# Performance work log

Hardware: AMD Instinct MI355X
Metric: run time of the kernel (lower is better)

The kernel has to match this reference:

```python
import jax, jax.numpy as jnp
import numpy as np

S, B, E, H, V, L = 128, 64, 512, 1024, 10000, 2


def setup_inputs() -> dict:
    key = jax.random.key(0)
    ks = jax.random.split(key, 10)
    s = 0.02  # weight scale ~ uniform(-k,k) magnitude
    return {
        "inputs": jax.random.randint(ks[0], (S, B), 0, V),
        "hidden": jnp.zeros((L, B, H), jnp.float32),
        "emb": jax.random.normal(ks[1], (V, E), jnp.float32) * 0.1,
        "Wx0": jax.random.normal(ks[2], (3, H, E), jnp.float32) * s,
        "Uh0": jax.random.normal(ks[3], (3, H, H), jnp.float32) * s,
        "b0": jax.random.normal(ks[4], (3, H), jnp.float32) * s,
        "Wx1": jax.random.normal(ks[5], (3, H, H), jnp.float32) * s,
        "Uh1": jax.random.normal(ks[6], (3, H, H), jnp.float32) * s,
        "b1": jax.random.normal(ks[7], (3, H), jnp.float32) * s,
        "Wd": jax.random.normal(ks[8], (V, H), jnp.float32) * 0.1,
        "bd": jnp.zeros((V,), jnp.float32),
    }


def _gru_cell(xp, h, U, b):
    # xp: (3,B,H) precomputed input projections in [r,z,h] order
    r = jax.nn.sigmoid(xp[0] + h @ U[0].T + b[0])
    z = jax.nn.sigmoid(xp[1] + h @ U[1].T + b[1])
    h_tilde = jnp.tanh(xp[2] + (r * h) @ U[2].T + b[2])
    return (1.0 - z) * h + z * h_tilde


def reference(inputs, hidden, emb, Wx0, Uh0, b0, Wx1, Uh1, b1, Wd, bd):
    x_embs = emb[inputs]                                   # [S,B,E]
    # precompute layer-0 input projections across all timesteps
    xa0 = jnp.einsum("sbe,goe->sgbo", x_embs, Wx0)        # [S,3,B,H]

    def step(carry, xa0_t):
        h0, h1 = carry
        h0n = _gru_cell(xa0_t, h0, Uh0, b0)
        xp1 = jnp.einsum("bk,gok->gbo", h0n, Wx1)          # [3,B,H]
        h1n = _gru_cell(xp1, h1, Uh1, b1)
        return (h0n, h1n), h1n

    (h0f, h1f), hs1 = jax.lax.scan(step, (hidden[0], hidden[1]), xa0)
    logits = jnp.einsum("sbh,vh->sbv", hs1, Wd) + bd       # [S,B,V]
    return logits, jnp.stack([h0f, h1f])
```

## Files before the change

kernel.cpp:

```cpp
#include <hip/hip_runtime.h>
#include <hip/hip_bf16.h>

#define SLEN 128
#define BAT 64
#define EDIM 512
#define HDIM 1024
#define VOC 10000
#define VPAD 10112
#define NWG_REC 256
#define TPB_REC 512

typedef short v8s __attribute__((ext_vector_type(8)));
typedef float v4f __attribute__((ext_vector_type(4)));
typedef unsigned short u16;

__device__ __forceinline__ u16 f2bf(float f) {
  unsigned u = __float_as_uint(f);
  u += 0x7fffu + ((u >> 16) & 1u);
  return (u16)(u >> 16);
}
__device__ __forceinline__ float bf2f(u16 b) {
  return __uint_as_float(((unsigned)b) << 16);
}
__device__ __forceinline__ float sigm(float x) { return 1.f / (1.f + __expf(-x)); }
__device__ __forceinline__ float tanh_f(float x) { return 1.f - 2.f / (1.f + __expf(2.f * x)); }

__device__ __forceinline__ void st_f32(float* p, float v) {
  __hip_atomic_store(p, v, __ATOMIC_RELAXED, __HIP_MEMORY_SCOPE_AGENT);
}
__device__ __forceinline__ float ld_f32(const float* p) {
  return __hip_atomic_load(p, __ATOMIC_RELAXED, __HIP_MEMORY_SCOPE_AGENT);
}
__device__ __forceinline__ float ld_bf16(const unsigned* base, int elem) {
  unsigned pr = __hip_atomic_load(base + (elem >> 1), __ATOMIC_RELAXED, __HIP_MEMORY_SCOPE_AGENT);
  return bf2f((u16)((elem & 1) ? (pr >> 16) : (pr & 0xffffu)));
}
__device__ __forceinline__ void st_bf16_pair(unsigned* base, int elem, u16 val, int l) {
  unsigned p = (unsigned)__shfl_xor((int)val, 1);
  if ((l & 1) == 0)
    __hip_atomic_store(base + (elem >> 1), (unsigned)val | (p << 16),
                       __ATOMIC_RELAXED, __HIP_MEMORY_SCOPE_AGENT);
}

__device__ __forceinline__ v4f gemm_staged(const char* Asrc, char* stage,
                                           const char* bb, int swz,
                                           int t, int rg, int lr, int lk2) {
  const char* gp = Asrc + (t >> 3) * 2048 + (t & 7) * 16;
  char* wp = stage + (t >> 3) * 128 + (((t & 7) * 16) ^ (((t >> 3) & 7) << 4));
  const char* rp = stage + (rg * 16 + lr) * 128;
  v4f acc{0.f, 0.f, 0.f, 0.f};
  v8s sreg[3];
  asm volatile("global_load_dwordx4 %0, %1, off sc0 sc1" : "=v"(sreg[0]) : "v"(gp));
  asm volatile("global_load_dwordx4 %0, %1, off offset:128 sc0 sc1" : "=v"(sreg[1]) : "v"(gp));
  asm volatile("global_load_dwordx4 %0, %1, off offset:256 sc0 sc1" : "=v"(sreg[2]) : "v"(gp));
  asm volatile("s_waitcnt vmcnt(2)" ::: "memory");
  __builtin_amdgcn_sched_barrier(0);
  *(v8s*)wp = sreg[0];
  __syncthreads();
#pragma unroll
  for (int c = 0; c < 16; ++c) {
    if (c < 13)
      asm volatile("global_load_dwordx4 %0, %1, off offset:%2 sc0 sc1"
                   : "=v"(sreg[c % 3]) : "v"(gp), "i"((c + 3) * 128));
    if (c < 15) {
      if (c < 13)       asm volatile("s_waitcnt vmcnt(2)" ::: "memory");
      else if (c == 13) asm volatile("s_waitcnt vmcnt(1)" ::: "memory");
      else              asm volatile("s_waitcnt vmcnt(0)" ::: "memory");
      __builtin_amdgcn_sched_barrier(0);
      *(v8s*)(wp + ((c + 1) & 1) * 8192) = sreg[(c + 1) % 3];
    }
    const char* buf = rp + (c & 1) * 8192;
#pragma unroll
    for (int ls = 0; ls < 2; ++ls) {
      v8s a = *(const v8s*)(buf + ((ls * 64 + lk2) ^ swz));
      v8s b = *(const v8s*)(bb + (((c * 2 + ls) * 64 + lk2) ^ swz));
      acc = __builtin_amdgcn_mfma_f32_16x16x32_bf16(a, b, acc, 0, 0, 0);
    }
    __syncthreads();
  }
  return acc;
}

#define POLL(COND)                                   \
  do {                                               \
    if (t < 64) {                                    \
      for (;;) {                                     \
        bool ok_ = (COND);                           \
        if (__all(ok_)) break;                       \
        __builtin_amdgcn_s_sleep(1);                 \
      }                                              \
    }                                                \
    __syncthreads();                                 \
  } while (0)

#define FENCE_FLAG(FIDX)                                                        \
  do {                                                                          \
    asm volatile("s_waitcnt vmcnt(0) lgkmcnt(0)" ::: "memory");                 \
    __syncthreads();                                                            \
    if (t == 0)                                                                 \
      __hip_atomic_store(&bar[FIDX], T + 1, __ATOMIC_RELAXED,                   \
                         __HIP_MEMORY_SCOPE_AGENT);                             \
  } while (0)

__global__ void __launch_bounds__(TPB_REC, 2) k_recur(
    const u16* __restrict__ Uh0b, const u16* __restrict__ Wx1b, const u16* __restrict__ Uh1b,
    const float* __restrict__ b0, const float* __restrict__ b1,
    const u16* __restrict__ xa0,
    float* __restrict__ h0f, u16* __restrict__ h0b,
    float* __restrict__ h1f, u16* __restrict__ h1b,
    u16* __restrict__ a2, float* __restrict__ z0,
    u16* __restrict__ a5, float* __restrict__ z1,
    u16* __restrict__ xp1,
    u16* __restrict__ hs1,
    float* __restrict__ outh,
    int* __restrict__ bar) {
  extern __shared__ char smem[];
  const int wg = blockIdx.x;
  const int t = threadIdx.x;
  const int w = t >> 6;
  const int l = t & 63;
  const int lr = l & 15;
  const int lk2 = (l >> 4) * 16;
  const int rg = w >> 1, cg = w & 1;
  const int rbase = rg * 16 + ((l >> 4) << 2);
  const int swz = (lr & 7) << 4;
  char* stage = smem + 131072;

  unsigned* a2u  = (unsigned*)a2;
  unsigned* a5u  = (unsigned*)a5;
  unsigned* h0bu = (unsigned*)h0b;
  unsigned* h1bu = (unsigned*)h1b;
  unsigned* xpu  = (unsigned*)xp1;

  auto lf = [&](int i) {
    return __hip_atomic_load(&bar[i], __ATOMIC_RELAXED, __HIP_MEMORY_SCOPE_AGENT);
  };

  {
    const u16* w1src; int w1row0;
    if (wg < 64)       { w1src = Uh0b; w1row0 = wg * 32; }
    else if (wg < 96)  { w1src = Uh0b; w1row0 = 2048 + (wg - 64) * 32; }
    else if (wg < 192) { w1src = Wx1b; w1row0 = (wg - 96) * 32; }
    else               { w1src = Uh1b; w1row0 = (wg - 192) * 32; }
    for (int i = t; i < 4096; i += TPB_REC) {
      int c = i >> 7, j = i & 127;
      v8s v = *(const v8s*)(w1src + (size_t)(w1row0 + c) * HDIM + j * 8);
      *(v8s*)(smem + c * 2048 + ((j * 16) ^ ((c & 7) << 4))) = v;
    }
    if (wg >= 64 && wg < 96) {
      int w2row0 = 2048 + (wg - 64) * 32;
      for (int i = t; i < 4096; i += TPB_REC) {
        int c = i >> 7, j = i & 127;
        v8s v = *(const v8s*)(Uh1b + (size_t)(w2row0 + c) * HDIM + j * 8);
        *(v8s*)(smem + 65536 + c * 2048 + ((j * 16) ^ ((c & 7) << 4))) = v;
      }
    }
    __syncthreads();
  }

  const char* bb1 = smem + (cg * 16 + lr) * 2048;
  const char* bb2 = smem + 65536 + (cg * 16 + lr) * 2048;

  if (wg < 64) {
    const int g = wg >> 5;
    const int o = (wg * 32 + cg * 16 + lr) & 1023;
    const float bias = b0[g * HDIM + o];
    for (int T = 0; T <= SLEN + 1; ++T) {
      if (T < SLEN) {
        if (T >= 1) POLL(lf(64 + (t & 31)) >= T);
        const int pr = (T - 1) & 1, pw = T & 1;
        float xv[4], hv[4];
#pragma unroll
        for (int r = 0; r < 4; ++r) {
          int b = rbase + r;
          xv[r] = bf2f(xa0[((T * 3 + g) * BAT + b) * HDIM + o]);
          if (g == 0) hv[r] = ld_f32(h0f + pr * 65536 + b * HDIM + o);
        }
        v4f acc = gemm_staged((const char*)(h0b + pr * 65536), stage, bb1, swz, t, rg, lr, lk2);
#pragma unroll
        for (int r = 0; r < 4; ++r) {
          int b = rbase + r;
          float s = sigm(acc[r] + xv[r] + bias);
          if (g == 0) st_bf16_pair(a2u + pw * 32768, b * HDIM + o, f2bf(s * hv[r]), l);
          else        st_f32(z0 + pw * 65536 + b * HDIM + o, s);
        }
      }
      FENCE_FLAG(wg);
    }
  } else if (wg < 96) {
    const int j = wg - 64;
    const int o = j * 32 + cg * 16 + lr;
    const float bias0 = b0[2 * HDIM + o];
    const float bias1 = b1[2 * HDIM + o];
    for (int T = 0; T <= SLEN + 1; ++T) {
      if (T < SLEN) {
        POLL(lf(t & 31) >= T + 1);
        const int pr = (T - 1) & 1, pw = T & 1;
        float xv[4], hv[4];
#pragma unroll
        for (int r = 0; r < 4; ++r) {
          int b = rbase + r;
          xv[r] = bf2f(xa0[((T * 3 + 2) * BAT + b) * HDIM + o]);
          hv[r] = ld_f32(h0f + pr * 65536 + b * HDIM + o);
        }
        v4f acc = gemm_staged((const char*)(a2 + pw * 65536), stage, bb1, swz, t, rg, lr, lk2);
        POLL(lf(32 + (t & 31)) >= T + 1 && lf(128 + t) >= T && lf(192 + (t & 31)) >= T);
        float zv[4];
#pragma unroll
        for (int r = 0; r < 4; ++r) zv[r] = ld_f32(z0 + pw * 65536 + (rbase + r) * HDIM + o);
#pragma unroll
        for (int r = 0; r < 4; ++r) {
          int b = rbase + r;
          float ht = tanh_f(xv[r] + acc[r] + bias0);
          float hn = (1.f - zv[r]) * hv[r] + zv[r] * ht;
          st_f32(h0f + pw * 65536 + b * HDIM + o, hn);
          st_bf16_pair(h0bu + pw * 32768, b * HDIM + o, f2bf(hn), l);
          if (T == SLEN - 1) outh[b * HDIM + o] = hn;
        }
      }
      FENCE_FLAG(64 + j);
      if (T >= 2) {
        const int t5 = T - 2, p5 = t5 & 1, pm = (T - 3) & 1;
        POLL(lf(224 + t) >= T + 1);
        v4f acc = gemm_staged((const char*)(a5 + p5 * 65536), stage, bb2, swz, t, rg, lr, lk2);
        float pv[4], zv[4], hv[4];
#pragma unroll
        for (int r = 0; r < 4; ++r) {
          int b = rbase + r;
          pv[r] = ld_bf16(xpu + p5 * 98304, b * 3072 + 2048 + o);
          zv[r] = ld_f32(z1 + p5 * 65536 + b * HDIM + o);
          hv[r] = ld_f32(h1f + pm * 65536 + b * HDIM + o);
        }
#pragma unroll
        for (int r = 0; r < 4; ++r) {
          int b = rbase + r;
          float ht = tanh_f(pv[r] + acc[r] + bias1);
          float hn = (1.f - zv[r]) * hv[r] + zv[r] * ht;
          u16 hb = f2bf(hn);
          st_f32(h1f + p5 * 65536 + b * HDIM + o, hn);
          st_bf16_pair(h1bu + p5 * 32768, b * HDIM + o, hb, l);
          hs1[((size_t)t5 * BAT + b) * HDIM + o] = hb;
          if (t5 == SLEN - 1) outh[(size_t)BAT * HDIM + b * HDIM + o] = hn;
        }
      }
      FENCE_FLAG(96 + j);
    }
  } else if (wg < 192) {
    const int j = wg - 96;
    const int n = j * 32 + cg * 16 + lr;
    for (int T = 0; T <= SLEN + 1; ++T) {
      if (T >= 1 && T <= SLEN) {
        POLL(lf(64 + (t & 31)) >= T && lf(96 + (t & 31)) >= T);
        const int ts = T - 1, ps = ts & 1;
        v4f acc = gemm_staged((const char*)(h0b + ps * 65536), stage, bb1, swz, t, rg, lr, lk2);
        unsigned* xp = xpu + ps * 98304;
#pragma unroll
        for (int r = 0; r < 4; ++r)
          st_bf16_pair(xp, (rbase + r) * 3072 + n, f2bf(acc[r]), l);
      }
      FENCE_FLAG(128 + j);
    }
  } else {
    const int j = wg - 192;
    const int g = j >> 5;
    const int o = (j * 32 + cg * 16 + lr) & 1023;
    const float bias = b1[g * HDIM + o];
    for (int T = 0; T <= SLEN + 1; ++T) {
      if (T >= 2) {
        POLL(lf(96 + (t & 31)) >= T);
        const int ts = T - 2, ps = ts & 1, pm = (T - 3) & 1;
        v4f acc = gemm_staged((const char*)(h1b + pm * 65536), stage, bb1, swz, t, rg, lr, lk2);
        POLL(lf(128 + t) >= T && lf(192 + (t & 31)) >= T);
        float pv[4], hv[4];
#pragma unroll
        for (int r = 0; r < 4; ++r) {
          int b = rbase + r;
          pv[r] = ld_bf16(xpu + ps * 98304, b * 3072 + g * HDIM + o);
          if (g == 0) hv[r] = ld_f32(h1f + pm * 65536 + b * HDIM + o);
        }
#pragma unroll
        for (int r = 0; r < 4; ++r) {
          int b = rbase + r;
          float s = sigm(acc[r] + pv[r] + bias);
          if (g == 0) st_bf16_pair(a5u + ps * 32768, b * HDIM + o, f2bf(s * hv[r]), l);
          else        st_f32(z1 + ps * 65536 + b * HDIM + o, s);
        }
      }
      FENCE_FLAG(224 + j);
    }
  }
}

template <int MODE>
__global__ void __launch_bounds__(256) k_gemm(
    const u16* __restrict__ A, const u16* __restrict__ Bw,
    const int* __restrict__ gidx, const float* __restrict__ bias,
    void* __restrict__ Out) {
  constexpr int K = MODE ? 1024 : 512;
  constexpr int NB_N = MODE ? (VPAD / 128) : (3072 / 128);

  __shared__ u16 sA[128 * 64];
  __shared__ u16 sB[128 * 64];

  const int nwg = gridDim.x;
  const int cpx = nwg >> 3;
  const int bid = blockIdx.x;
  const int swz = (bid & 7) * cpx + (bid >> 3);
  const int bm = swz / NB_N, bn = swz % NB_N;
  const int m0 = bm * 128, n0 = bn * 128;

  const int t = threadIdx.x;
  const int w = t >> 6, l = t & 63;
  const int lr = l & 15, lk = (l >> 4) * 8;
  const int wm = (w >> 1) * 64, wn = (w & 1) * 64;
  const int kc = (t & 7) * 8;

  int arowg[4];
#pragma unroll
  for (int i = 0; i < 4; ++i) {
    int row = m0 + i * 32 + (t >> 3);
    arowg[i] = (MODE == 0) ? gidx[row] : row;
  }
  int brow[4];
#pragma unroll
  for (int i = 0; i < 4; ++i) brow[i] = n0 + i * 32 + (t >> 3);

  v4f acc[4][4];
#pragma unroll
  for (int mi = 0; mi < 4; ++mi)
#pragma unroll
    for (int ni = 0; ni < 4; ++ni) acc[mi][ni] = v4f{0.f, 0.f, 0.f, 0.f};

  for (int k0 = 0; k0 < K; k0 += 64) {
    __syncthreads();
#pragma unroll
    for (int i = 0; i < 4; ++i) {
      const u16* src = A + (size_t)arowg[i] * K + k0 + kc;
      __builtin_amdgcn_global_load_lds((const __attribute__((address_space(1))) void*)src,
                                       (__attribute__((address_space(3))) void*)(sA + i * 2048 + w * 512),
                                       16, 0, 0);
    }
#pragma unroll
    for (int i = 0; i < 4; ++i) {
      const u16* src = Bw + (size_t)brow[i] * K + k0 + kc;
      __builtin_amdgcn_global_load_lds((const __attribute__((address_space(1))) void*)src,
                                       (__attribute__((address_space(3))) void*)(sB + i * 2048 + w * 512),
                                       16, 0, 0);
    }
    asm volatile("s_waitcnt vmcnt(0)" ::: "memory");
    __syncthreads();
#pragma unroll
    for (int ks = 0; ks < 2; ++ks) {
      v8s af[4], bfr[4];
#pragma unroll
      for (int mi = 0; mi < 4; ++mi) af[mi] = *(const v8s*)&sA[(wm + mi * 16 + lr) * 64 + ks * 32 + lk];
#pragma unroll
      for (int ni = 0; ni < 4; ++ni) bfr[ni] = *(const v8s*)&sB[(wn + ni * 16 + lr) * 64 + ks * 32 + lk];
#pragma unroll
      for (int mi = 0; mi < 4; ++mi)
#pragma unroll
        for (int ni = 0; ni < 4; ++ni)
          acc[mi][ni] = __builtin_amdgcn_mfma_f32_16x16x32_bf16(af[mi], bfr[ni], acc[mi][ni], 0, 0, 0);
    }
  }

#pragma unroll
  for (int mi = 0; mi < 4; ++mi)
#pragma unroll
    for (int ni = 0; ni < 4; ++ni)
#pragma unroll
      for (int r = 0; r < 4; ++r) {
        int grow = m0 + wm + mi * 16 + ((l >> 4) << 2) + r;
        int gcol = n0 + wn + ni * 16 + lr;
        float v = acc[mi][ni][r];
        if (MODE == 0) {
          int s = grow >> 6, b = grow & 63;
          int g = gcol >> 10, o = gcol & 1023;
          ((u16*)Out)[(((size_t)s * 3 + g) * BAT + b) * HDIM + o] = f2bf(v);
        } else {
          if (gcol < VOC) ((float*)Out)[(size_t)grow * VOC + gcol] = v + bias[gcol];
        }
      }
}

__global__ void k_cvt(const float* __restrict__ src, u16* __restrict__ dst, int n, int nsrc) {
  int i = (blockIdx.x * 256 + threadIdx.x) * 4;
  if (i >= n) return;
#pragma unroll
  for (int j = 0; j < 4; ++j) {
    int idx = i + j;
    if (idx < n) dst[idx] = (idx < nsrc) ? f2bf(src[idx]) : (u16)0;
  }
}

__global__ void k_init(const float* __restrict__ hidden,
                       float* h0f, u16* h0b, float* h1f, u16* h1b, int* bar) {
  int i = blockIdx.x * 256 + threadIdx.x;
  if (i < BAT * HDIM) {
    float v0 = hidden[i];
    float v1 = hidden[BAT * HDIM + i];
    h0f[65536 + i] = v0; h0b[65536 + i] = f2bf(v0);
    h1f[65536 + i] = v1; h1b[65536 + i] = f2bf(v1);
  }
  if (i < 512) bar[i] = 0;
}

extern "C" void kernel_launch(void* const* d_in, const int* in_sizes, int n_in,
                              void* d_out, int out_size, void* d_ws, size_t ws_size,
                              hipStream_t stream) {
  const int*   inp = (const int*)d_in[0];
  const float* hid = (const float*)d_in[1];
  const float* emb = (const float*)d_in[2];
  const float* Wx0 = (const float*)d_in[3];
  const float* Uh0 = (const float*)d_in[4];
  const float* b0  = (const float*)d_in[5];
  const float* Wx1 = (const float*)d_in[6];
  const float* Uh1 = (const float*)d_in[7];
  const float* b1  = (const float*)d_in[8];
  const float* Wd  = (const float*)d_in[9];
  const float* bd  = (const float*)d_in[10];

  char* ws = (char*)d_ws;
  size_t off = 0;
  auto alloc = [&](size_t bytes) {
    void* p = ws + off;
    off = (off + bytes + 255) & ~(size_t)255;
    return p;
  };
  u16* emb_b = (u16*)alloc(sizeof(u16) * (size_t)VOC * EDIM);
  u16* Wx0_b = (u16*)alloc(sizeof(u16) * 3 * HDIM * EDIM);
  u16* Uh0_b = (u16*)alloc(sizeof(u16) * 3 * HDIM * HDIM);
  u16* Wx1_b = (u16*)alloc(sizeof(u16) * 3 * HDIM * HDIM);
  u16* Uh1_b = (u16*)alloc(sizeof(u16) * 3 * HDIM * HDIM);
  u16* Wd_b  = (u16*)alloc(sizeof(u16) * (size_t)VPAD * HDIM);
  u16* xa0_b = (u16*)alloc(sizeof(u16) * (size_t)SLEN * 3 * BAT * HDIM);
  u16* hs1_b = (u16*)alloc(sizeof(u16) * (size_t)SLEN * BAT * HDIM);
  u16* xp1   = (u16*)alloc(sizeof(u16) * 2 * BAT * 3 * HDIM);
  float* h0f = (float*)alloc(sizeof(float) * 2 * BAT * HDIM);
  float* h1f = (float*)alloc(sizeof(float) * 2 * BAT * HDIM);
  u16* h0b   = (u16*)alloc(sizeof(u16) * 2 * BAT * HDIM);
  u16* h1b   = (u16*)alloc(sizeof(u16) * 2 * BAT * HDIM);
  u16* a2    = (u16*)alloc(sizeof(u16) * 2 * BAT * HDIM);
  u16* a5    = (u16*)alloc(sizeof(u16) * 2 * BAT * HDIM);
  float* z0  = (float*)alloc(sizeof(float) * 2 * BAT * HDIM);
  float* z1  = (float*)alloc(sizeof(float) * 2 * BAT * HDIM);
  int* bar   = (int*)alloc(sizeof(int) * 512);

  float* logits = (float*)d_out;
  float* outh = logits + (size_t)SLEN * BAT * VOC;

  auto cvt = [&](const float* s, u16* d, int n, int nsrc) {
    k_cvt<<<dim3((n / 4 + 255) / 256), dim3(256), 0, stream>>>(s, d, n, nsrc);
  };
  cvt(emb, emb_b, VOC * EDIM, VOC * EDIM);
  cvt(Wx0, Wx0_b, 3 * HDIM * EDIM, 3 * HDIM * EDIM);
  cvt(Uh0, Uh0_b, 3 * HDIM * HDIM, 3 * HDIM * HDIM);
  cvt(Wx1, Wx1_b, 3 * HDIM * HDIM, 3 * HDIM * HDIM);
  cvt(Uh1, Uh1_b, 3 * HDIM * HDIM, 3 * HDIM * HDIM);
  cvt(Wd, Wd_b, VPAD * HDIM, VOC * HDIM);
  k_init<<<dim3(256), dim3(256), 0, stream>>>(hid, h0f, h0b, h1f, h1b, bar);

  k_gemm<0><<<dim3(64 * 24), dim3(256), 0, stream>>>(emb_b, Wx0_b, inp, (const float*)nullptr, (void*)xa0_b);

  (void)hipFuncSetAttribute(reinterpret_cast<const void*>(k_recur),
                            hipFuncAttributeMaxDynamicSharedMemorySize, 147456);
  k_recur<<<dim3(NWG_REC), dim3(TPB_REC), 147456, stream>>>(
      Uh0_b, Wx1_b, Uh1_b, b0, b1, xa0_b,
      h0f, h0b, h1f, h1b, a2, z0, a5, z1, xp1, hs1_b, outh, bar);

  k_gemm<1><<<dim3(64 * 79), dim3(256), 0, stream>>>(hs1_b, Wd_b, (const int*)nullptr, bd, d_out);
}
```

Baseline: 2.880 ms.

## Repartition persistent GRU recurrence onto 144 workgroups with 64-column weight tiles

The persistent recurrent kernel is repartitioned so each workgroup owns 64 output columns (two MFMA accumulators per wave) instead of 32. That cuts the grid from 256 to 144 workgroups, and the layer-1 candidate gate now gets its own dedicated workgroups rather than sharing the layer-0 ones. The staging pipeline for the activation operand is deepened from 3 to 5 in-flight loads, and the flag dependencies between stages are rewired. The aim is fewer workgroups to poll and synchronise per step and more MFMA work per activation load, at the cost of larger per-workgroup weight tiles in LDS and longer per-step compute on each workgroup.

```diff
diff --git a/kernel.cpp b/kernel.cpp
--- a/kernel.cpp
+++ b/kernel.cpp
@@ -7,7 +7,7 @@
 #define HDIM 1024
 #define VOC 10000
 #define VPAD 10112
-#define NWG_REC 256
+#define NWG_REC 144
 #define TPB_REC 512
 
 typedef short v8s __attribute__((ext_vector_type(8)));
@@ -40,45 +40,6 @@
   if ((l & 1) == 0)
     __hip_atomic_store(base + (elem >> 1), (unsigned)val | (p << 16),
                        __ATOMIC_RELAXED, __HIP_MEMORY_SCOPE_AGENT);
-}
-
-__device__ __forceinline__ v4f gemm_staged(const char* Asrc, char* stage,
-                                           const char* bb, int swz,
-                                           int t, int rg, int lr, int lk2) {
-  const char* gp = Asrc + (t >> 3) * 2048 + (t & 7) * 16;
-  char* wp = stage + (t >> 3) * 128 + (((t & 7) * 16) ^ (((t >> 3) & 7) << 4));
-  const char* rp = stage + (rg * 16 + lr) * 128;
-  v4f acc{0.f, 0.f, 0.f, 0.f};
-  v8s sreg[3];
-  asm volatile("global_load_dwordx4 %0, %1, off sc0 sc1" : "=v"(sreg[0]) : "v"(gp));
-  asm volatile("global_load_dwordx4 %0, %1, off offset:128 sc0 sc1" : "=v"(sreg[1]) : "v"(gp));
-  asm volatile("global_load_dwordx4 %0, %1, off offset:256 sc0 sc1" : "=v"(sreg[2]) : "v"(gp));
-  asm volatile("s_waitcnt vmcnt(2)" ::: "memory");
-  __builtin_amdgcn_sched_barrier(0);
-  *(v8s*)wp = sreg[0];
-  __syncthreads();
-#pragma unroll
-  for (int c = 0; c < 16; ++c) {
-    if (c < 13)
-      asm volatile("global_load_dwordx4 %0, %1, off offset:%2 sc0 sc1"
-                   : "=v"(sreg[c % 3]) : "v"(gp), "i"((c + 3) * 128));
-    if (c < 15) {
-      if (c < 13)       asm volatile("s_waitcnt vmcnt(2)" ::: "memory");
-      else if (c == 13) asm volatile("s_waitcnt vmcnt(1)" ::: "memory");
-      else              asm volatile("s_waitcnt vmcnt(0)" ::: "memory");
-      __builtin_amdgcn_sched_barrier(0);
-      *(v8s*)(wp + ((c + 1) & 1) * 8192) = sreg[(c + 1) % 3];
-    }
-    const char* buf = rp + (c & 1) * 8192;
-#pragma unroll
-    for (int ls = 0; ls < 2; ++ls) {
-      v8s a = *(const v8s*)(buf + ((ls * 64 + lk2) ^ swz));
-      v8s b = *(const v8s*)(bb + (((c * 2 + ls) * 64 + lk2) ^ swz));
-      acc = __builtin_amdgcn_mfma_f32_16x16x32_bf16(a, b, acc, 0, 0, 0);
-    }
-    __syncthreads();
-  }
-  return acc;
 }
 
 #define POLL(COND)                                   \
@@ -101,6 +62,45 @@
       __hip_atomic_store(&bar[FIDX], T + 1, __ATOMIC_RELAXED,                   \
                          __HIP_MEMORY_SCOPE_AGENT);                             \
   } while (0)
+
+__device__ __forceinline__ void gemm64(const char* Asrc, char* stage,
+                                       const char* bb, int swz,
+                                       int t, int rg, int lr, int lk2,
+                                       v4f& acc0, v4f& acc1) {
+  const char* gp = Asrc + (t >> 3) * 2048 + (t & 7) * 16;
+  char* wp = stage + (t >> 3) * 128 + (((t & 7) * 16) ^ (((t >> 3) & 7) << 4));
+  const char* rp = stage + (rg * 16 + lr) * 128;
+  v8s sreg[5];
+#pragma unroll
+  for (int j = 0; j < 5; ++j)
+    asm volatile("global_load_dwordx4 %0, %1, off offset:%2 sc0 sc1"
+                 : "=v"(sreg[j]) : "v"(gp), "i"(j * 128));
+  asm volatile("s_waitcnt vmcnt(4)" ::: "memory");
+  __builtin_amdgcn_sched_barrier(0);
+  *(v8s*)wp = sreg[0];
+  __syncthreads();
+#pragma unroll
+  for (int c = 0; c < 16; ++c) {
+    if (c < 11)
+      asm volatile("global_load_dwordx4 %0, %1, off offset:%2 sc0 sc1"
+                   : "=v"(sreg[c % 5]) : "v"(gp), "i"((c + 5) * 128));
+    if (c < 15) {
+      asm volatile("s_waitcnt vmcnt(%0)" :: "i"((c < 11) ? 4 : (14 - c)));
+      __builtin_amdgcn_sched_barrier(0);
+      *(v8s*)(wp + ((c + 1) & 1) * 8192) = sreg[(c + 1) % 5];
+    }
+    const char* buf = rp + (c & 1) * 8192;
+#pragma unroll
+    for (int ls = 0; ls < 2; ++ls) {
+      v8s a = *(const v8s*)(buf + ((ls * 64 + lk2) ^ swz));
+      v8s b0v = *(const v8s*)(bb + (((c * 2 + ls) * 64 + lk2) ^ swz));
+      v8s b1v = *(const v8s*)(bb + 32768 + (((c * 2 + ls) * 64 + lk2) ^ swz));
+      acc0 = __builtin_amdgcn_mfma_f32_16x16x32_bf16(a, b0v, acc0, 0, 0, 0);
+      acc1 = __builtin_amdgcn_mfma_f32_16x16x32_bf16(a, b1v, acc1, 0, 0, 0);
+    }
+    __syncthreads();
+  }
+}
 
 __global__ void __launch_bounds__(TPB_REC, 2) k_recur(
     const u16* __restrict__ Uh0b, const u16* __restrict__ Wx1b, const u16* __restrict__ Uh1b,
@@ -137,156 +137,203 @@
   };
 
   {
-    const u16* w1src; int w1row0;
-    if (wg < 64)       { w1src = Uh0b; w1row0 = wg * 32; }
-    else if (wg < 96)  { w1src = Uh0b; w1row0 = 2048 + (wg - 64) * 32; }
-    else if (wg < 192) { w1src = Wx1b; w1row0 = (wg - 96) * 32; }
-    else               { w1src = Uh1b; w1row0 = (wg - 192) * 32; }
-    for (int i = t; i < 4096; i += TPB_REC) {
+    const u16* wsrc; int wrow0;
+    if (wg < 32)       { wsrc = Uh0b; wrow0 = wg * 64; }
+    else if (wg < 48)  { wsrc = Uh0b; wrow0 = 2048 + (wg - 32) * 64; }
+    else if (wg < 96)  { wsrc = Wx1b; wrow0 = (wg - 48) * 64; }
+    else if (wg < 128) { wsrc = Uh1b; wrow0 = (wg - 96) * 64; }
+    else               { wsrc = Uh1b; wrow0 = 2048 + (wg - 128) * 64; }
+    for (int i = t; i < 8192; i += TPB_REC) {
       int c = i >> 7, j = i & 127;
-      v8s v = *(const v8s*)(w1src + (size_t)(w1row0 + c) * HDIM + j * 8);
+      v8s v = *(const v8s*)(wsrc + (size_t)(wrow0 + c) * HDIM + j * 8);
       *(v8s*)(smem + c * 2048 + ((j * 16) ^ ((c & 7) << 4))) = v;
     }
-    if (wg >= 64 && wg < 96) {
-      int w2row0 = 2048 + (wg - 64) * 32;
-      for (int i = t; i < 4096; i += TPB_REC) {
-        int c = i >> 7, j = i & 127;
-        v8s v = *(const v8s*)(Uh1b + (size_t)(w2row0 + c) * HDIM + j * 8);
-        *(v8s*)(smem + 65536 + c * 2048 + ((j * 16) ^ ((c & 7) << 4))) = v;
-      }
-    }
     __syncthreads();
   }
 
-  const char* bb1 = smem + (cg * 16 + lr) * 2048;
-  const char* bb2 = smem + 65536 + (cg * 16 + lr) * 2048;
-
-  if (wg < 64) {
-    const int g = wg >> 5;
-    const int o = (wg * 32 + cg * 16 + lr) & 1023;
-    const float bias = b0[g * HDIM + o];
+  const char* bb = smem + (cg * 32 + lr) * 2048;
+
+  if (wg < 32) {
+    const int g = wg >> 4;
+    const int o0 = ((wg * 64) & 1023) + cg * 32 + lr;
+    const float biasA0 = b0[g * HDIM + o0];
+    const float biasA1 = b0[g * HDIM + o0 + 16];
     for (int T = 0; T <= SLEN + 1; ++T) {
       if (T < SLEN) {
-        if (T >= 1) POLL(lf(64 + (t & 31)) >= T);
+        if (T >= 1) POLL(lf(32 + (t & 15)) >= T);
         const int pr = (T - 1) & 1, pw = T & 1;
-        float xv[4], hv[4];
-#pragma unroll
-        for (int r = 0; r < 4; ++r) {
-          int b = rbase + r;
-          xv[r] = bf2f(xa0[((T * 3 + g) * BAT + b) * HDIM + o]);
-          if (g == 0) hv[r] = ld_f32(h0f + pr * 65536 + b * HDIM + o);
-        }
-        v4f acc = gemm_staged((const char*)(h0b + pr * 65536), stage, bb1, swz, t, rg, lr, lk2);
-#pragma unroll
-        for (int r = 0; r < 4; ++r) {
-          int b = rbase + r;
-          float s = sigm(acc[r] + xv[r] + bias);
-          if (g == 0) st_bf16_pair(a2u + pw * 32768, b * HDIM + o, f2bf(s * hv[r]), l);
-          else        st_f32(z0 + pw * 65536 + b * HDIM + o, s);
+        float xv[2][4], hv[2][4];
+#pragma unroll
+        for (int f = 0; f < 2; ++f) {
+          const int o = o0 + f * 16;
+#pragma unroll
+          for (int r = 0; r < 4; ++r) {
+            int b = rbase + r;
+            xv[f][r] = bf2f(xa0[((T * 3 + g) * BAT + b) * HDIM + o]);
+            if (g == 0) hv[f][r] = ld_f32(h0f + pr * 65536 + b * HDIM + o);
+          }
+        }
+        v4f acc0{0.f,0.f,0.f,0.f}, acc1{0.f,0.f,0.f,0.f};
+        gemm64((const char*)(h0b + pr * 65536), stage, bb, swz, t, rg, lr, lk2, acc0, acc1);
+#pragma unroll
+        for (int f = 0; f < 2; ++f) {
+          const int o = o0 + f * 16;
+          const float bias = f ? biasA1 : biasA0;
+          v4f& acc = f ? acc1 : acc0;
+#pragma unroll
+          for (int r = 0; r < 4; ++r) {
+            int b = rbase + r;
+            float s = sigm(acc[r] + xv[f][r] + bias);
+            if (g == 0) st_bf16_pair(a2u + pw * 32768, b * HDIM + o, f2bf(s * hv[f][r]), l);
+            else        st_f32(z0 + pw * 65536 + b * HDIM + o, s);
+          }
         }
       }
       FENCE_FLAG(wg);
     }
-  } else if (wg < 96) {
-    const int j = wg - 64;
-    const int o = j * 32 + cg * 16 + lr;
-    const float bias0 = b0[2 * HDIM + o];
-    const float bias1 = b1[2 * HDIM + o];
+  } else if (wg < 48) {
+    const int j = wg - 32;
+    const int o0 = j * 64 + cg * 32 + lr;
+    const float biasB0 = b0[2 * HDIM + o0];
+    const float biasB1 = b0[2 * HDIM + o0 + 16];
     for (int T = 0; T <= SLEN + 1; ++T) {
       if (T < SLEN) {
         POLL(lf(t & 31) >= T + 1);
         const int pr = (T - 1) & 1, pw = T & 1;
-        float xv[4], hv[4];
-#pragma unroll
-        for (int r = 0; r < 4; ++r) {
-          int b = rbase + r;
-          xv[r] = bf2f(xa0[((T * 3 + 2) * BAT + b) * HDIM + o]);
-          hv[r] = ld_f32(h0f + pr * 65536 + b * HDIM + o);
-        }
-        v4f acc = gemm_staged((const char*)(a2 + pw * 65536), stage, bb1, swz, t, rg, lr, lk2);
-        POLL(lf(32 + (t & 31)) >= T + 1 && lf(128 + t) >= T && lf(192 + (t & 31)) >= T);
-        float zv[4];
-#pragma unroll
-        for (int r = 0; r < 4; ++r) zv[r] = ld_f32(z0 + pw * 65536 + (rbase + r) * HDIM + o);
-#pragma unroll
-        for (int r = 0; r < 4; ++r) {
-          int b = rbase + r;
-          float ht = tanh_f(xv[r] + acc[r] + bias0);
-          float hn = (1.f - zv[r]) * hv[r] + zv[r] * ht;
-          st_f32(h0f + pw * 65536 + b * HDIM + o, hn);
-          st_bf16_pair(h0bu + pw * 32768, b * HDIM + o, f2bf(hn), l);
-          if (T == SLEN - 1) outh[b * HDIM + o] = hn;
+        float xv[2][4], hv[2][4], zv[2][4];
+#pragma unroll
+        for (int f = 0; f < 2; ++f) {
+          const int o = o0 + f * 16;
+#pragma unroll
+          for (int r = 0; r < 4; ++r) {
+            int b = rbase + r;
+            xv[f][r] = bf2f(xa0[((T * 3 + 2) * BAT + b) * HDIM + o]);
+            hv[f][r] = ld_f32(h0f + pr * 65536 + b * HDIM + o);
+            zv[f][r] = ld_f32(z0 + pw * 65536 + b * HDIM + o);
+          }
+        }
+        v4f acc0{0.f,0.f,0.f,0.f}, acc1{0.f,0.f,0.f,0.f};
+        gemm64((const char*)(a2 + pw * 65536), stage, bb, swz, t, rg, lr, lk2, acc0, acc1);
+        POLL(t < 48 ? lf(48 + t) >= T : true);
+#pragma unroll
+        for (int f = 0; f < 2; ++f) {
+          const int o = o0 + f * 16;
+          const float bias = f ? biasB1 : biasB0;
+          v4f& acc = f ? acc1 : acc0;
+#pragma unroll
+          for (int r = 0; r < 4; ++r) {
+            int b = rbase + r;
+            float ht = tanh_f(xv[f][r] + acc[r] + bias);
+            float hn = (1.f - zv[f][r]) * hv[f][r] + zv[f][r] * ht;
+            st_f32(h0f + pw * 65536 + b * HDIM + o, hn);
+            st_bf16_pair(h0bu + pw * 32768, b * HDIM + o, f2bf(hn), l);
+            if (T == SLEN - 1) outh[b * HDIM + o] = hn;
+          }
         }
       }
-      FENCE_FLAG(64 + j);
+      FENCE_FLAG(32 + j);
+    }
+  } else if (wg < 96) {
+    const int j = wg - 48;
+    const int n0 = j * 64 + cg * 32 + lr;
+    for (int T = 0; T <= SLEN + 1; ++T) {
+      if (T >= 1 && T <= SLEN) {
+        POLL(lf(32 + (t & 15)) >= T);
+        const int ps = (T - 1) & 1;
+        v4f acc0{0.f,0.f,0.f,0.f}, acc1{0.f,0.f,0.f,0.f};
+        gemm64((const char*)(h0b + ps * 65536), stage, bb, swz, t, rg, lr, lk2, acc0, acc1);
+        POLL(lf(96 + (t & 31)) >= T && lf(128 + (t & 15)) >= T);
+        unsigned* xp = xpu + ps * 98304;
+#pragma unroll
+        for (int f = 0; f < 2; ++f) {
+          const int n = n0 + f * 16;
+          v4f& acc = f ? acc1 : acc0;
+#pragma unroll
+          for (int r = 0; r < 4; ++r)
+            st_bf16_pair(xp, (rbase + r) * 3072 + n, f2bf(acc[r]), l);
+        }
+      }
+      FENCE_FLAG(48 + j);
+    }
+  } else if (wg < 128) {
+    const int j = wg - 96;
+    const int g = j >> 4;
+    const int o0 = ((j * 64) & 1023) + cg * 32 + lr;
+    const float biasD0 = b1[g * HDIM + o0];
+    const float biasD1 = b1[g * HDIM + o0 + 16];
+    for (int T = 0; T <= SLEN + 1; ++T) {
       if (T >= 2) {
-        const int t5 = T - 2, p5 = t5 & 1, pm = (T - 3) & 1;
-        POLL(lf(224 + t) >= T + 1);
-        v4f acc = gemm_staged((const char*)(a5 + p5 * 65536), stage, bb2, swz, t, rg, lr, lk2);
-        float pv[4], zv[4], hv[4];
-#pragma unroll
-        for (int r = 0; r < 4; ++r) {
-          int b = rbase + r;
-          pv[r] = ld_bf16(xpu + p5 * 98304, b * 3072 + 2048 + o);
-          zv[r] = ld_f32(z1 + p5 * 65536 + b * HDIM + o);
-          hv[r] = ld_f32(h1f + pm * 65536 + b * HDIM + o);
-        }
-#pragma unroll
-        for (int r = 0; r < 4; ++r) {
-          int b = rbase + r;
-          float ht = tanh_f(pv[r] + acc[r] + bias1);
-          float hn = (1.f - zv[r]) * hv[r] + zv[r] * ht;
-          u16 hb = f2bf(hn);
-          st_f32(h1f + p5 * 65536 + b * HDIM + o, hn);
-          st_bf16_pair(h1bu + p5 * 32768, b * HDIM + o, hb, l);
-          hs1[((size_t)t5 * BAT + b) * HDIM + o] = hb;
-          if (t5 == SLEN - 1) outh[(size_t)BAT * HDIM + b * HDIM + o] = hn;
+        POLL(lf(128 + (t & 15)) >= T);
+        const int s = T - 2, ps = s & 1, pm = (T - 1) & 1;
+        float hv[2][4];
+        if (g == 0)
+#pragma unroll
+          for (int f = 0; f < 2; ++f)
+#pragma unroll
+            for (int r = 0; r < 4; ++r)
+              hv[f][r] = ld_f32(h1f + pm * 65536 + (rbase + r) * HDIM + o0 + f * 16);
+        v4f acc0{0.f,0.f,0.f,0.f}, acc1{0.f,0.f,0.f,0.f};
+        gemm64((const char*)(h1b + pm * 65536), stage, bb, swz, t, rg, lr, lk2, acc0, acc1);
+        POLL(t < 48 ? lf(48 + t) >= T : true);
+#pragma unroll
+        for (int f = 0; f < 2; ++f) {
+          const int o = o0 + f * 16;
+          const float bias = f ? biasD1 : biasD0;
+          v4f& acc = f ? acc1 : acc0;
+#pragma unroll
+          for (int r = 0; r < 4; ++r) {
+            int b = rbase + r;
+            float pv = ld_bf16(xpu + ps * 98304, b * 3072 + g * HDIM + o);
+            float sg = sigm(acc[r] + pv + bias);
+            if (g == 0) st_bf16_pair(a5u + ps * 32768, b * HDIM + o, f2bf(sg * hv[f][r]), l);
+            else        st_f32(z1 + ps * 65536 + b * HDIM + o, sg);
+          }
         }
       }
       FENCE_FLAG(96 + j);
     }
-  } else if (wg < 192) {
-    const int j = wg - 96;
-    const int n = j * 32 + cg * 16 + lr;
+  } else {
+    const int j = wg - 128;
+    const int o0 = j * 64 + cg * 32 + lr;
+    const float biasE0 = b1[2 * HDIM + o0];
+    const float biasE1 = b1[2 * HDIM + o0 + 16];
     for (int T = 0; T <= SLEN + 1; ++T) {
-      if (T >= 1 && T <= SLEN) {
-        POLL(lf(64 + (t & 31)) >= T && lf(96 + (t & 31)) >= T);
-        const int ts = T - 1, ps = ts & 1;
-        v4f acc = gemm_staged((const char*)(h0b + ps * 65536), stage, bb1, swz, t, rg, lr, lk2);
-        unsigned* xp = xpu + ps * 98304;
-#pragma unroll
-        for (int r = 0; r < 4; ++r)
-          st_bf16_pair(xp, (rbase + r) * 3072 + n, f2bf(acc[r]), l);
+      if (T >= 2) {
+        POLL(lf(96 + (t & 31)) >= T + 1);
+        const int s = T - 2, ps = s & 1, pm = (T - 1) & 1;
+        float pv[2][4], zv[2][4], hv[2][4];
+#pragma unroll
+        for (int f = 0; f < 2; ++f) {
+          const int o = o0 + f * 16;
+#pragma unroll
+          for (int r = 0; r < 4; ++r) {
+            int b = rbase + r;
+            pv[f][r] = ld_bf16(xpu + ps * 98304, b * 3072 + 2048 + o);
+            zv[f][r] = ld_f32(z1 + ps * 65536 + b * HDIM + o);
+            hv[f][r] = ld_f32(h1f + pm * 65536 + b * HDIM + o);
+          }
+        }
+        v4f acc0{0.f,0.f,0.f,0.f}, acc1{0.f,0.f,0.f,0.f};
+        gemm64((const char*)(a5 + ps * 65536), stage, bb, swz, t, rg, lr, lk2, acc0, acc1);
+#pragma unroll
+        for (int f = 0; f < 2; ++f) {
+          const int o = o0 + f * 16;
+          const float bias = f ? biasE1 : biasE0;
+          v4f& acc = f ? acc1 : acc0;
+#pragma unroll
+          for (int r = 0; r < 4; ++r) {
+            int b = rbase + r;
+            float ht = tanh_f(pv[f][r] + acc[r] + bias);
+            float hn = (1.f - zv[f][r]) * hv[f][r] + zv[f][r] * ht;
+            u16 hb = f2bf(hn);
+            st_f32(h1f + ps * 65536 + b * HDIM + o, hn);
+            st_bf16_pair(h1bu + ps * 32768, b * HDIM + o, hb, l);
+            hs1[((size_t)s * BAT + b) * HDIM + o] = hb;
+            if (s == SLEN - 1) outh[(size_t)BAT * HDIM + b * HDIM + o] = hn;
+          }
+        }
       }
       FENCE_FLAG(128 + j);
-    }
-  } else {
-    const int j = wg - 192;
-    const int g = j >> 5;
-    const int o = (j * 32 + cg * 16 + lr) & 1023;
-    const float bias = b1[g * HDIM + o];
-    for (int T = 0; T <= SLEN + 1; ++T) {
-      if (T >= 2) {
-        POLL(lf(96 + (t & 31)) >= T);
-        const int ts = T - 2, ps = ts & 1, pm = (T - 3) & 1;
-        v4f acc = gemm_staged((const char*)(h1b + pm * 65536), stage, bb1, swz, t, rg, lr, lk2);
-        POLL(lf(128 + t) >= T && lf(192 + (t & 31)) >= T);
-        float pv[4], hv[4];
-#pragma unroll
-        for (int r = 0; r < 4; ++r) {
-          int b = rbase + r;
-          pv[r] = ld_bf16(xpu + ps * 98304, b * 3072 + g * HDIM + o);
-          if (g == 0) hv[r] = ld_f32(h1f + pm * 65536 + b * HDIM + o);
-        }
-#pragma unroll
-        for (int r = 0; r < 4; ++r) {
-          int b = rbase + r;
-          float s = sigm(acc[r] + pv[r] + bias);
-          if (g == 0) st_bf16_pair(a5u + ps * 32768, b * HDIM + o, f2bf(s * hv[r]), l);
-          else        st_f32(z1 + ps * 65536 + b * HDIM + o, s);
-        }
-      }
-      FENCE_FLAG(224 + j);
     }
   }
 }
```

Result: slower. 3.176 ms (+10.3%).
